# Kernel optimization log

Measured on AMD Instinct MI355X. Metric: run time of the kernel, lower is better.

## Reference

```python
import jax, jax.numpy as jnp
import numpy as np

LEAK = 0.2
N, C, T, H, DOUT = 512, 16, 15, 32, 32


def setup_inputs() -> dict:
    key = jax.random.key(0)
    k = jax.random.split(key, 5)
    x = jax.random.normal(k[0], (N, C), dtype=jnp.float32)
    adj = jax.random.uniform(k[1], (N, N, T), dtype=jnp.float32)
    W1 = jax.random.normal(k[2], (2 * C, T + 1, H), dtype=jnp.float32) * 0.05
    W2 = jax.random.normal(k[3], (2 * C, T + 1, DOUT), dtype=jnp.float32) * 0.05
    W3 = jax.random.normal(k[4], (C, H), dtype=jnp.float32) * 0.05
    return {"x": x, "adj": adj, "W1": W1, "W2": W2, "W3": W3}


def reference(x, adj, W1, W2, W3):
    n, c = x.shape
    # input_diag: [N,N,C,1], diagonal copy of node features
    diag = jnp.einsum('mn,ni->mni', jnp.eye(n, dtype=x.dtype), x)[..., None]
    # D = concat(adj-weighted broadcast of x, diag) along edge-type axis -> [N,N,C,T+1]
    D = jnp.concatenate([jnp.einsum('mnt,ni->mnit', adj, x), diag], axis=3)
    # symmetrize along channel axis -> [N,N,2C,T+1]
    D = jnp.concatenate([D, jnp.transpose(D, (1, 0, 2, 3))], axis=2)
    K = jnp.einsum('mnit,ith->mnh', D, W1)   # [N,N,H]
    V = jnp.einsum('mnit,itd->mnd', D, W2)   # [N,N,DOUT]
    Q = x @ W3                               # [N,H]
    logits1 = jnp.einsum('nh,nmh->nm', Q, K)
    logits2 = jnp.einsum('mh,nmh->nm', Q, K)
    s1 = jax.nn.softmax(logits1, axis=1)
    s2 = jax.nn.softmax(logits2, axis=0)
    temp = jnp.einsum('nm,nmd->nd', s1, V) + jnp.einsum('nm,nmd->md', s2, V)
    return jnp.maximum(temp, LEAK * temp)  # lrelu
```

## Files before the change

kernel.cpp:

```cpp
#include <hip/hip_runtime.h>
#include <hip/hip_bf16.h>

#define NNODE 512
#define CCH   16
#define TT    15
#define TP    16
#define HH    32
#define DD    32

typedef unsigned short u16;
typedef unsigned int   u32;
typedef short bf8 __attribute__((ext_vector_type(8)));
typedef float f4  __attribute__((ext_vector_type(4)));

__device__ __forceinline__ float bf2f(u16 v) {
    union { u32 u; float f; } x; x.u = ((u32)v) << 16; return x.f;
}
__device__ __forceinline__ u16 f2bf(float f) {
    union { float f; u32 u; } x; x.f = f;
    u32 u = x.u;
    return (u16)((u + 0x7FFFu + ((u >> 16) & 1u)) >> 16);
}
__device__ __forceinline__ void unpack8(uint4 p, float* o) {
    o[0]=bf2f((u16)(p.x & 0xffffu)); o[1]=bf2f((u16)(p.x >> 16));
    o[2]=bf2f((u16)(p.y & 0xffffu)); o[3]=bf2f((u16)(p.y >> 16));
    o[4]=bf2f((u16)(p.z & 0xffffu)); o[5]=bf2f((u16)(p.z >> 16));
    o[6]=bf2f((u16)(p.w & 0xffffu)); o[7]=bf2f((u16)(p.w >> 16));
}
__device__ __forceinline__ uint4 pack8(const u16* v) {
    return make_uint4((u32)v[0]|((u32)v[1]<<16), (u32)v[2]|((u32)v[3]<<16),
                      (u32)v[4]|((u32)v[5]<<16), (u32)v[6]|((u32)v[7]<<16));
}

__global__ __launch_bounds__(256) void k_prep_adjp(
    const float* __restrict__ x, const float* __restrict__ W1,
    const float* __restrict__ W2, const float* __restrict__ W3,
    const float* __restrict__ adj,
    u16* __restrict__ A1, u16* __restrict__ B1,
    u16* __restrict__ A2T, u16* __restrict__ B2T,
    u16* __restrict__ Qb, float* __restrict__ QAd, float* __restrict__ QB,
    u16* __restrict__ adjP, u16* __restrict__ adjPT)
{
    int tid = threadIdx.x;
    if (blockIdx.x < 512) {
        int n = blockIdx.x;
        __shared__ alignas(16) float xs[CCH];
        __shared__ alignas(16) float A1row[512], B1row[512];
        __shared__ alignas(16) float A2row[512], B2row[512];
        __shared__ alignas(16) float Qs[HH];
        if (tid < CCH) xs[tid] = x[n*CCH + tid];
        __syncthreads();
        float xr[CCH];
        #pragma unroll
        for (int i=0;i<CCH;i++) xr[i]=xs[i];
        #pragma unroll
        for (int rep=0; rep<2; rep++) {
            int c = tid + rep*256;
            float a1=0.f,b1=0.f,a2=0.f,b2=0.f;
            #pragma unroll
            for (int i=0;i<CCH;i++) {
                a1 += xr[i]*W1[i*512 + c];
                b1 += xr[i]*W1[(CCH+i)*512 + c];
                a2 += xr[i]*W2[i*512 + c];
                b2 += xr[i]*W2[(CCH+i)*512 + c];
            }
            A1[(size_t)n*512 + c]=f2bf(a1); B1[(size_t)n*512 + c]=f2bf(b1);
            A1row[c]=a1; B1row[c]=b1; A2row[c]=a2; B2row[c]=b2;
        }
        if (tid < HH) {
            float q=0.f;
            #pragma unroll
            for (int i=0;i<CCH;i++) q += xr[i]*W3[i*HH + tid];
            Qs[tid]=q; Qb[(size_t)n*HH + tid]=f2bf(q);
        }
        __syncthreads();
        if (tid < TP) {
            float qa=0.f, qb=0.f;
            #pragma unroll
            for (int h=0;h<HH;h++) { qa += Qs[h]*A1row[tid*HH+h]; qb += Qs[h]*B1row[tid*HH+h]; }
            QAd[(size_t)n*TP + tid]=qa; QB[(size_t)n*TP + tid]=qb;
        }
        {
            int d = tid >> 3, t0 = (tid & 7) * 2;
            u32 pa = (u32)f2bf(A2row[t0*32 + d]) | ((u32)f2bf(A2row[(t0+1)*32 + d]) << 16);
            u32 pb = (u32)f2bf(B2row[t0*32 + d]) | ((u32)f2bf(B2row[(t0+1)*32 + d]) << 16);
            *(u32*)(A2T + (size_t)d*8192 + n*16 + t0) = pa;
            *(u32*)(B2T + (size_t)d*8192 + n*16 + t0) = pb;
        }
    } else {
        int b = blockIdx.x - 512;
        int n0 = (b >> 4) * 32, m0 = (b & 15) * 32;
        __shared__ alignas(16) u16 s[32*520];
        #pragma unroll
        for (int i = 0; i < 60; i++) {
            int e = tid + i*256;
            int nl = e / 480; int rem = e - nl*480;
            int ml = rem / 15; int t = rem - ml*15;
            float v = adj[((size_t)(n0+nl)*512 + (m0+ml))*TT + t];
            s[nl*520 + ml*16 + t] = f2bf(v);
        }
        #pragma unroll
        for (int i = 0; i < 4; i++) {
            int e = tid + i*256; int nl = e >> 5, ml = e & 31;
            s[nl*520 + ml*16 + 15] = ((n0+nl) == (m0+ml)) ? (u16)0x3F80 : (u16)0;
        }
        __syncthreads();
        #pragma unroll
        for (int i = 0; i < 8; i++) {
            int c = tid + i*256;
            int nl = c >> 6, off = (c & 63) * 8;
            uint4 vv = *(const uint4*)(s + nl*520 + off);
            *(uint4*)(adjP + (size_t)(n0+nl)*8192 + m0*16 + off) = vv;
        }
        #pragma unroll
        for (int i = 0; i < 8; i++) {
            int c = tid + i*256;
            int ml = c >> 6, nlh = c & 63, nl = nlh >> 1, half = nlh & 1;
            uint4 vv = *(const uint4*)(s + nl*520 + ml*16 + half*8);
            *(uint4*)(adjPT + (size_t)(m0+ml)*8192 + (n0+nl)*16 + half*8) = vv;
        }
    }
}

__global__ __launch_bounds__(256) void k_logits(
    const u16* __restrict__ Qb, const u16* __restrict__ A1, const u16* __restrict__ B1,
    const u16* __restrict__ adjP, const u16* __restrict__ adjPT,
    const float* __restrict__ QAd, const float* __restrict__ QB,
    float* __restrict__ L1, float* __restrict__ L2T)
{
    const int m0 = blockIdx.x * 16, n0 = blockIdx.y * 16;
    const int tid = threadIdx.x;
    const int wv = tid >> 6, lane = tid & 63, l15 = lane & 15, quad = lane >> 4;
    __shared__ alignas(16) float sL1[16*17];
    __shared__ alignas(16) float sL2[16*17];

    bf8 qbN = *(const bf8*)(Qb + (size_t)(n0 + l15)*32 + quad*8);
    bf8 qbM = *(const bf8*)(Qb + (size_t)(m0 + l15)*32 + quad*8);
    float4 qb4 = *(const float4*)(QB  + (size_t)(n0 + l15)*TP + quad*4);
    float4 qa4 = *(const float4*)(QAd + (size_t)(m0 + l15)*TP + quad*4);

    #pragma unroll
    for (int j = 0; j < 4; j++) {
        int m = m0 + wv*4 + j;
        bf8 aA1 = *(const bf8*)(A1 + (size_t)m*512 + l15*32 + quad*8);
        f4 z = {0.f,0.f,0.f,0.f};
        f4 g = __builtin_amdgcn_mfma_f32_16x16x32_bf16(aA1, qbN, z, 0, 0, 0);
        uint2 ax = *(const uint2*)(adjPT + (size_t)m*8192 + (n0 + l15)*16 + quad*4);
        uint2 ay = *(const uint2*)(adjP  + (size_t)m*8192 + (n0 + l15)*16 + quad*4);
        float v;
        v = bf2f((u16)(ax.x & 0xffffu)) * g[0];
        v = fmaf(bf2f((u16)(ax.x >> 16)),     g[1], v);
        v = fmaf(bf2f((u16)(ax.y & 0xffffu)), g[2], v);
        v = fmaf(bf2f((u16)(ax.y >> 16)),     g[3], v);
        v = fmaf(bf2f((u16)(ay.x & 0xffffu)), qb4.x, v);
        v = fmaf(bf2f((u16)(ay.x >> 16)),     qb4.y, v);
        v = fmaf(bf2f((u16)(ay.y & 0xffffu)), qb4.z, v);
        v = fmaf(bf2f((u16)(ay.y >> 16)),     qb4.w, v);
        v += __shfl_xor(v, 16, 64);
        v += __shfl_xor(v, 32, 64);
        if (quad == 0) sL1[l15*17 + wv*4 + j] = v;
    }
    #pragma unroll
    for (int j = 0; j < 4; j++) {
        int n = n0 + wv*4 + j;
        bf8 aB1 = *(const bf8*)(B1 + (size_t)n*512 + l15*32 + quad*8);
        f4 z = {0.f,0.f,0.f,0.f};
        f4 h = __builtin_amdgcn_mfma_f32_16x16x32_bf16(aB1, qbM, z, 0, 0, 0);
        uint2 ax = *(const uint2*)(adjPT + (size_t)n*8192 + (m0 + l15)*16 + quad*4);
        uint2 ay = *(const uint2*)(adjP  + (size_t)n*8192 + (m0 + l15)*16 + quad*4);
        float v;
        v = bf2f((u16)(ax.x & 0xffffu)) * h[0];
        v = fmaf(bf2f((u16)(ax.x >> 16)),     h[1], v);
        v = fmaf(bf2f((u16)(ax.y & 0xffffu)), h[2], v);
        v = fmaf(bf2f((u16)(ax.y >> 16)),     h[3], v);
        v = fmaf(bf2f((u16)(ay.x & 0xffffu)), qa4.x, v);
        v = fmaf(bf2f((u16)(ay.x >> 16)),     qa4.y, v);
        v = fmaf(bf2f((u16)(ay.y & 0xffffu)), qa4.z, v);
        v = fmaf(bf2f((u16)(ay.y >> 16)),     qa4.w, v);
        v += __shfl_xor(v, 16, 64);
        v += __shfl_xor(v, 32, 64);
        if (quad == 0) sL2[l15*17 + wv*4 + j] = v;
    }
    __syncthreads();
    int row = tid >> 4, col = tid & 15;
    L1 [(size_t)(n0+row)*NNODE + m0 + col] = sL1[row*17+col];
    L2T[(size_t)(m0+row)*NNODE + n0 + col] = sL2[row*17+col];
}

__global__ __launch_bounds__(256) void k_smx_gemm(
    const float* __restrict__ L1, const float* __restrict__ L2T,
    const u16* __restrict__ adjP, const u16* __restrict__ adjPT,
    const u16* __restrict__ A2T, const u16* __restrict__ B2T,
    float* __restrict__ tempP2, float* __restrict__ uP)
{
    const int j0 = blockIdx.x * 16, kc = blockIdx.y, dir = blockIdx.z;
    const int tid = threadIdx.x;
    const int wv = tid >> 6, lane = tid & 63, l15 = lane & 15, quad = lane >> 4;
    const float* Lbase = dir ? L2T : L1;

    __shared__ alignas(16) u16 Wt[16*512];
    __shared__ alignas(16) float redb[4][512];
    __shared__ float mxs[16], invs[16];

    #pragma unroll
    for (int rr = 0; rr < 4; rr++) {
        int jr = wv*4 + rr;
        const float* rw = Lbase + (size_t)(j0 + jr)*NNODE;
        float4 a = *(const float4*)(rw + lane*8);
        float4 b = *(const float4*)(rw + lane*8 + 4);
        float mx = fmaxf(fmaxf(fmaxf(a.x,a.y),fmaxf(a.z,a.w)),
                         fmaxf(fmaxf(b.x,b.y),fmaxf(b.z,b.w)));
        #pragma unroll
        for (int o=32; o; o>>=1) mx = fmaxf(mx, __shfl_xor(mx, o, 64));
        float sm = __expf(a.x-mx)+__expf(a.y-mx)+__expf(a.z-mx)+__expf(a.w-mx)
                 + __expf(b.x-mx)+__expf(b.y-mx)+__expf(b.z-mx)+__expf(b.w-mx);
        #pragma unroll
        for (int o=32; o; o>>=1) sm += __shfl_xor(sm, o, 64);
        if (lane == 0) { mxs[jr] = mx; invs[jr] = 1.0f/sm; }
    }
    __syncthreads();

    {
        int j = tid >> 4, cb = tid & 15;
        float mxj = mxs[j], invj = invs[j];
        int mg = kc*32 + cb*2;
        const float* rw = Lbase + (size_t)(j0 + j)*NNODE;
        float s0 = __expf(rw[mg]   - mxj) * invj;
        float s1 = __expf(rw[mg+1] - mxj) * invj;

        const uint4* pp = (const uint4*)(adjP + (size_t)(j0+j)*8192 + kc*512 + cb*32);
        float av[32];
        unpack8(pp[0], av); unpack8(pp[1], av+8); unpack8(pp[2], av+16); unpack8(pp[3], av+24);
        u16 wo[32];
        #pragma unroll
        for (int e=0;e<16;e++) wo[e]    = f2bf(s0*av[e]);
        #pragma unroll
        for (int e=0;e<16;e++) wo[16+e] = f2bf(s1*av[16+e]);
        #pragma unroll
        for (int q=0;q<4;q++) {
            int sl = (cb*4 + q) ^ (j & 7);
            *(uint4*)&Wt[j*512 + sl*8] = pack8(wo + q*8);
        }

        const uint4* qq4 = (const uint4*)(adjPT + (size_t)(j0+j)*8192 + kc*512 + cb*32);
        float tv[32];
        unpack8(qq4[0], tv); unpack8(qq4[1], tv+8); unpack8(qq4[2], tv+16); unpack8(qq4[3], tv+24);
        float ut[16];
        #pragma unroll
        for (int t=0;t<16;t++) ut[t] = s0*tv[t] + s1*tv[16+t];
        #pragma unroll
        for (int i=0;i<8;i++) {
            float v0 = (lane&1) ? ut[i] : ut[i+8];
            float r0 = __shfl_xor(v0, 1, 64);
            ut[i] = ((lane&1) ? ut[i+8] : ut[i]) + r0;
        }
        #pragma unroll
        for (int i=0;i<4;i++) {
            float v0 = (lane&2) ? ut[i] : ut[i+4];
            float r0 = __shfl_xor(v0, 2, 64);
            ut[i] = ((lane&2) ? ut[i+4] : ut[i]) + r0;
        }
        #pragma unroll
        for (int i=0;i<2;i++) {
            float v0 = (lane&4) ? ut[i] : ut[i+2];
            float r0 = __shfl_xor(v0, 4, 64);
            ut[i] = ((lane&4) ? ut[i+2] : ut[i]) + r0;
        }
        {
            float v0 = (lane&8) ? ut[0] : ut[1];
            float r0 = __shfl_xor(v0, 8, 64);
            ut[0] = ((lane&8) ? ut[1] : ut[0]) + r0;
        }
        int tm = ((cb&1)<<3) | ((cb&2)<<1) | ((cb&4)>>1) | ((cb&8)>>3);
        uP[((size_t)(dir*16 + kc)*NNODE + j0 + j)*TP + tm] = ut[0];
    }
    __syncthreads();

    {
        const u16* Bmat = dir ? B2T : A2T;
        f4 acc0 = {0.f,0.f,0.f,0.f}, acc1 = {0.f,0.f,0.f,0.f};
        #pragma unroll
        for (int st = 0; st < 4; st++) {
            int s = wv*4 + st;
            bf8 afr = *(const bf8*)&Wt[l15*512 + (((s*4 + quad) ^ (l15 & 7)) << 3)];
            bf8 b0 = *(const bf8*)(Bmat + (size_t)(l15)*8192    + kc*512 + s*32 + quad*8);
            bf8 b1 = *(const bf8*)(Bmat + (size_t)(16+l15)*8192 + kc*512 + s*32 + quad*8);
            acc0 = __builtin_amdgcn_mfma_f32_16x16x32_bf16(afr, b0, acc0, 0, 0, 0);
            acc1 = __builtin_amdgcn_mfma_f32_16x16x32_bf16(afr, b1, acc1, 0, 0, 0);
        }
        #pragma unroll
        for (int r = 0; r < 4; r++) {
            redb[wv][      (quad*4+r)*16 + l15] = acc0[r];
            redb[wv][256 + (quad*4+r)*16 + l15] = acc1[r];
        }
    }
    __syncthreads();
    #pragma unroll
    for (int h = 0; h < 2; h++) {
        int o = tid + h*256;
        int jj = o >> 5, d = o & 31;
        int idx = (d >> 4)*256 + jj*16 + (d & 15);
        float v = redb[0][idx] + redb[1][idx] + redb[2][idx] + redb[3][idx];
        tempP2[(((size_t)dir*16 + kc)*NNODE + j0 + jj)*DD + d] = v;
    }
}

__global__ __launch_bounds__(256) void k_final(
    const float* __restrict__ tempP2, const float* __restrict__ uP,
    const u16* __restrict__ A2T, const u16* __restrict__ B2T, float* __restrict__ out)
{
    int blk = blockIdx.x, tid = threadIdx.x;
    int jbase = blk*8;
    __shared__ float u1L[8][16], v2L[8][16];
    {
        int dsel = tid >> 7;
        int i = tid & 127; int jj = i >> 4, t = i & 15;
        float s = 0.f;
        #pragma unroll
        for (int kcc = 0; kcc < 16; kcc++)
            s += uP[(((size_t)dsel*16 + kcc)*NNODE + jbase + jj)*TP + t];
        if (dsel) v2L[jj][t] = s; else u1L[jj][t] = s;
    }
    __syncthreads();
    int base = blk*256 + tid;
    int j = base >> 5, d = base & 31, jj = j & 7;
    float acc = 0.f;
    #pragma unroll
    for (int p = 0; p < 32; p++) acc += tempP2[((size_t)p*NNODE + j)*DD + d];
    const uint4* pb2 = (const uint4*)(B2T + (size_t)d*8192 + j*16);
    const uint4* pa2 = (const uint4*)(A2T + (size_t)d*8192 + j*16);
    float bv[16], avv[16];
    unpack8(pb2[0], bv);  unpack8(pb2[1], bv+8);
    unpack8(pa2[0], avv); unpack8(pa2[1], avv+8);
    #pragma unroll
    for (int t = 0; t < 16; t++)
        acc += u1L[jj][t]*bv[t] + v2L[jj][t]*avv[t];
    out[(size_t)j*DD + d] = fmaxf(acc, 0.2f*acc);
}

extern "C" void kernel_launch(void* const* d_in, const int* in_sizes, int n_in,
                              void* d_out, int out_size, void* d_ws, size_t ws_size,
                              hipStream_t stream)
{
    (void)in_sizes; (void)n_in; (void)out_size; (void)ws_size;
    const float* x   = (const float*)d_in[0];
    const float* adj = (const float*)d_in[1];
    const float* W1  = (const float*)d_in[2];
    const float* W2  = (const float*)d_in[3];
    const float* W3  = (const float*)d_in[4];

    char* ws = (char*)d_ws;
    u16*   adjP  = (u16*)(ws);
    u16*   adjPT = (u16*)(ws + 0x800000);
    u16*   A1    = (u16*)(ws + 0x1000000);
    u16*   B1    = (u16*)(ws + 0x1080000);
    u16*   A2T   = (u16*)(ws + 0x1100000);
    u16*   B2T   = (u16*)(ws + 0x1180000);
    u16*   Qb    = (u16*)(ws + 0x1200000);
    float* QAd   = (float*)(ws + 0x1210000);
    float* QB    = (float*)(ws + 0x1220000);
    float* L1    = (float*)(ws + 0x1300000);
    float* L2T   = (float*)(ws + 0x1400000);
    float* tempP2= (float*)(ws + 0x1500000);
    float* uP    = (float*)(ws + 0x1700000);

    k_prep_adjp<<<768, 256, 0, stream>>>(x, W1, W2, W3, adj,
                                         A1, B1, A2T, B2T, Qb, QAd, QB, adjP, adjPT);
    k_logits<<<dim3(32,32), 256, 0, stream>>>(Qb, A1, B1, adjP, adjPT, QAd, QB, L1, L2T);
    k_smx_gemm<<<dim3(32,16,2), 256, 0, stream>>>(L1, L2T, adjP, adjPT, A2T, B2T, tempP2, uP);
    k_final<<<64, 256, 0, stream>>>(tempP2, uP, A2T, B2T, (float*)d_out);
}
```

Measured before the change: 103.4 us.

## Split softmax stats into own kernel, double gemm grid, reduce partials with atomics

Moves the per-row softmax max and sum computation out of k_smx_gemm into a new k_stats kernel, which also zeroes the accumulators. k_smx_gemm then runs with half the K-chunk per block over twice as many blocks. Partial results are accumulated with float atomicAdd into temp/u1/v2, so k_final no longer sums 32 partial buffers. This removes redundant recomputation of row statistics in every block and the partial-sum reduction, at the cost of an extra launch, atomic contention, and non-deterministic summation order.

```diff
diff --git a/kernel.cpp b/kernel.cpp
--- a/kernel.cpp
+++ b/kernel.cpp
@@ -187,67 +187,75 @@
     L2T[(size_t)(m0+row)*NNODE + n0 + col] = sL2[row*17+col];
 }
 
+__global__ __launch_bounds__(256) void k_stats(
+    const float* __restrict__ L1, const float* __restrict__ L2T,
+    float2* __restrict__ stats, float* __restrict__ temp,
+    float* __restrict__ u1, float* __restrict__ v2)
+{
+    int tid = threadIdx.x;
+    int g0 = blockIdx.x * 256 + tid;
+    if (g0 < 16384) temp[g0] = 0.f;
+    else if (g0 < 24576) u1[g0 - 16384] = 0.f;
+    else if (g0 < 32768) v2[g0 - 24576] = 0.f;
+
+    int wv = tid >> 6, lane = tid & 63;
+    int g = blockIdx.x * 4 + wv;
+    const float* rw = (g < NNODE) ? (L1 + (size_t)g*NNODE)
+                                  : (L2T + (size_t)(g - NNODE)*NNODE);
+    float4 a = *(const float4*)(rw + lane*8);
+    float4 b = *(const float4*)(rw + lane*8 + 4);
+    float mx = fmaxf(fmaxf(fmaxf(a.x,a.y),fmaxf(a.z,a.w)),
+                     fmaxf(fmaxf(b.x,b.y),fmaxf(b.z,b.w)));
+    #pragma unroll
+    for (int o=32; o; o>>=1) mx = fmaxf(mx, __shfl_xor(mx, o, 64));
+    float sm = __expf(a.x-mx)+__expf(a.y-mx)+__expf(a.z-mx)+__expf(a.w-mx)
+             + __expf(b.x-mx)+__expf(b.y-mx)+__expf(b.z-mx)+__expf(b.w-mx);
+    #pragma unroll
+    for (int o=32; o; o>>=1) sm += __shfl_xor(sm, o, 64);
+    if (lane == 0) { float2 st; st.x = mx; st.y = 1.0f/sm; stats[g] = st; }
+}
+
 __global__ __launch_bounds__(256) void k_smx_gemm(
     const float* __restrict__ L1, const float* __restrict__ L2T,
     const u16* __restrict__ adjP, const u16* __restrict__ adjPT,
     const u16* __restrict__ A2T, const u16* __restrict__ B2T,
-    float* __restrict__ tempP2, float* __restrict__ uP)
+    const float2* __restrict__ stats,
+    float* __restrict__ temp, float* __restrict__ u1, float* __restrict__ v2)
 {
     const int j0 = blockIdx.x * 16, kc = blockIdx.y, dir = blockIdx.z;
     const int tid = threadIdx.x;
     const int wv = tid >> 6, lane = tid & 63, l15 = lane & 15, quad = lane >> 4;
     const float* Lbase = dir ? L2T : L1;
 
-    __shared__ alignas(16) u16 Wt[16*512];
+    __shared__ alignas(16) u16 Wt[16*256];
     __shared__ alignas(16) float redb[4][512];
-    __shared__ float mxs[16], invs[16];
-
-    #pragma unroll
-    for (int rr = 0; rr < 4; rr++) {
-        int jr = wv*4 + rr;
-        const float* rw = Lbase + (size_t)(j0 + jr)*NNODE;
-        float4 a = *(const float4*)(rw + lane*8);
-        float4 b = *(const float4*)(rw + lane*8 + 4);
-        float mx = fmaxf(fmaxf(fmaxf(a.x,a.y),fmaxf(a.z,a.w)),
-                         fmaxf(fmaxf(b.x,b.y),fmaxf(b.z,b.w)));
-        #pragma unroll
-        for (int o=32; o; o>>=1) mx = fmaxf(mx, __shfl_xor(mx, o, 64));
-        float sm = __expf(a.x-mx)+__expf(a.y-mx)+__expf(a.z-mx)+__expf(a.w-mx)
-                 + __expf(b.x-mx)+__expf(b.y-mx)+__expf(b.z-mx)+__expf(b.w-mx);
-        #pragma unroll
-        for (int o=32; o; o>>=1) sm += __shfl_xor(sm, o, 64);
-        if (lane == 0) { mxs[jr] = mx; invs[jr] = 1.0f/sm; }
-    }
+    __shared__ float2 sst[16];
+
+    if (tid < 16) sst[tid] = stats[dir*NNODE + j0 + tid];
     __syncthreads();
 
     {
         int j = tid >> 4, cb = tid & 15;
-        float mxj = mxs[j], invj = invs[j];
-        int mg = kc*32 + cb*2;
-        const float* rw = Lbase + (size_t)(j0 + j)*NNODE;
-        float s0 = __expf(rw[mg]   - mxj) * invj;
-        float s1 = __expf(rw[mg+1] - mxj) * invj;
-
-        const uint4* pp = (const uint4*)(adjP + (size_t)(j0+j)*8192 + kc*512 + cb*32);
-        float av[32];
-        unpack8(pp[0], av); unpack8(pp[1], av+8); unpack8(pp[2], av+16); unpack8(pp[3], av+24);
-        u16 wo[32];
-        #pragma unroll
-        for (int e=0;e<16;e++) wo[e]    = f2bf(s0*av[e]);
-        #pragma unroll
-        for (int e=0;e<16;e++) wo[16+e] = f2bf(s1*av[16+e]);
-        #pragma unroll
-        for (int q=0;q<4;q++) {
-            int sl = (cb*4 + q) ^ (j & 7);
-            *(uint4*)&Wt[j*512 + sl*8] = pack8(wo + q*8);
-        }
-
-        const uint4* qq4 = (const uint4*)(adjPT + (size_t)(j0+j)*8192 + kc*512 + cb*32);
-        float tv[32];
-        unpack8(qq4[0], tv); unpack8(qq4[1], tv+8); unpack8(qq4[2], tv+16); unpack8(qq4[3], tv+24);
+        int m = kc*16 + cb;
+        float2 st = sst[j];
+        float s0 = __expf(Lbase[(size_t)(j0+j)*NNODE + m] - st.x) * st.y;
+
+        const uint4* pp = (const uint4*)(adjP + (size_t)(j0+j)*8192 + m*16);
+        float av[16]; unpack8(pp[0], av); unpack8(pp[1], av+8);
+        u16 wo[16];
+        #pragma unroll
+        for (int e=0;e<16;e++) wo[e] = f2bf(s0*av[e]);
+        #pragma unroll
+        for (int q=0;q<2;q++) {
+            int sl = (cb*2 + q) ^ (j & 7);
+            *(uint4*)&Wt[j*256 + sl*8] = pack8(wo + q*8);
+        }
+
+        const uint4* qq = (const uint4*)(adjPT + (size_t)(j0+j)*8192 + m*16);
+        float tv[16]; unpack8(qq[0], tv); unpack8(qq[1], tv+8);
         float ut[16];
         #pragma unroll
-        for (int t=0;t<16;t++) ut[t] = s0*tv[t] + s1*tv[16+t];
+        for (int t=0;t<16;t++) ut[t] = s0*tv[t];
         #pragma unroll
         for (int i=0;i<8;i++) {
             float v0 = (lane&1) ? ut[i] : ut[i+8];
@@ -272,7 +280,7 @@
             ut[0] = ((lane&8) ? ut[1] : ut[0]) + r0;
         }
         int tm = ((cb&1)<<3) | ((cb&2)<<1) | ((cb&4)>>1) | ((cb&8)>>3);
-        uP[((size_t)(dir*16 + kc)*NNODE + j0 + j)*TP + tm] = ut[0];
+        atomicAdd((dir ? v2 : u1) + (size_t)(j0+j)*TP + tm, ut[0]);
     }
     __syncthreads();
 
@@ -280,11 +288,11 @@
         const u16* Bmat = dir ? B2T : A2T;
         f4 acc0 = {0.f,0.f,0.f,0.f}, acc1 = {0.f,0.f,0.f,0.f};
         #pragma unroll
-        for (int st = 0; st < 4; st++) {
-            int s = wv*4 + st;
-            bf8 afr = *(const bf8*)&Wt[l15*512 + (((s*4 + quad) ^ (l15 & 7)) << 3)];
-            bf8 b0 = *(const bf8*)(Bmat + (size_t)(l15)*8192    + kc*512 + s*32 + quad*8);
-            bf8 b1 = *(const bf8*)(Bmat + (size_t)(16+l15)*8192 + kc*512 + s*32 + quad*8);
+        for (int st2 = 0; st2 < 2; st2++) {
+            int s = wv*2 + st2;
+            bf8 afr = *(const bf8*)&Wt[l15*256 + (((s*4 + quad) ^ (l15 & 7)) << 3)];
+            bf8 b0 = *(const bf8*)(Bmat + (size_t)(l15)*8192    + kc*256 + s*32 + quad*8);
+            bf8 b1 = *(const bf8*)(Bmat + (size_t)(16+l15)*8192 + kc*256 + s*32 + quad*8);
             acc0 = __builtin_amdgcn_mfma_f32_16x16x32_bf16(afr, b0, acc0, 0, 0, 0);
             acc1 = __builtin_amdgcn_mfma_f32_16x16x32_bf16(afr, b1, acc1, 0, 0, 0);
         }
@@ -301,32 +309,17 @@
         int jj = o >> 5, d = o & 31;
         int idx = (d >> 4)*256 + jj*16 + (d & 15);
         float v = redb[0][idx] + redb[1][idx] + redb[2][idx] + redb[3][idx];
-        tempP2[(((size_t)dir*16 + kc)*NNODE + j0 + jj)*DD + d] = v;
+        atomicAdd(&temp[(size_t)(j0 + jj)*DD + d], v);
     }
 }
 
 __global__ __launch_bounds__(256) void k_final(
-    const float* __restrict__ tempP2, const float* __restrict__ uP,
+    const float* __restrict__ temp, const float* __restrict__ u1, const float* __restrict__ v2,
     const u16* __restrict__ A2T, const u16* __restrict__ B2T, float* __restrict__ out)
 {
-    int blk = blockIdx.x, tid = threadIdx.x;
-    int jbase = blk*8;
-    __shared__ float u1L[8][16], v2L[8][16];
-    {
-        int dsel = tid >> 7;
-        int i = tid & 127; int jj = i >> 4, t = i & 15;
-        float s = 0.f;
-        #pragma unroll
-        for (int kcc = 0; kcc < 16; kcc++)
-            s += uP[(((size_t)dsel*16 + kcc)*NNODE + jbase + jj)*TP + t];
-        if (dsel) v2L[jj][t] = s; else u1L[jj][t] = s;
-    }
-    __syncthreads();
-    int base = blk*256 + tid;
-    int j = base >> 5, d = base & 31, jj = j & 7;
-    float acc = 0.f;
-    #pragma unroll
-    for (int p = 0; p < 32; p++) acc += tempP2[((size_t)p*NNODE + j)*DD + d];
+    int base = blockIdx.x * 256 + threadIdx.x;
+    int j = base >> 5, d = base & 31;
+    float acc = temp[(size_t)j*DD + d];
     const uint4* pb2 = (const uint4*)(B2T + (size_t)d*8192 + j*16);
     const uint4* pa2 = (const uint4*)(A2T + (size_t)d*8192 + j*16);
     float bv[16], avv[16];
@@ -334,7 +327,7 @@
     unpack8(pa2[0], avv); unpack8(pa2[1], avv+8);
     #pragma unroll
     for (int t = 0; t < 16; t++)
-        acc += u1L[jj][t]*bv[t] + v2L[jj][t]*avv[t];
+        acc += u1[(size_t)j*TP + t]*bv[t] + v2[(size_t)j*TP + t]*avv[t];
     out[(size_t)j*DD + d] = fmaxf(acc, 0.2f*acc);
 }
 
@@ -361,12 +354,16 @@
     float* QB    = (float*)(ws + 0x1220000);
     float* L1    = (float*)(ws + 0x1300000);
     float* L2T   = (float*)(ws + 0x1400000);
-    float* tempP2= (float*)(ws + 0x1500000);
-    float* uP    = (float*)(ws + 0x1700000);
+    float* temp  = (float*)(ws + 0x1500000);
+    float* u1    = (float*)(ws + 0x1510000);
+    float* v2    = (float*)(ws + 0x1520000);
+    float2* stats= (float2*)(ws + 0x1530000);
 
     k_prep_adjp<<<768, 256, 0, stream>>>(x, W1, W2, W3, adj,
                                          A1, B1, A2T, B2T, Qb, QAd, QB, adjP, adjPT);
     k_logits<<<dim3(32,32), 256, 0, stream>>>(Qb, A1, B1, adjP, adjPT, QAd, QB, L1, L2T);
-    k_smx_gemm<<<dim3(32,16,2), 256, 0, stream>>>(L1, L2T, adjP, adjPT, A2T, B2T, tempP2, uP);
-    k_final<<<64, 256, 0, stream>>>(tempP2, uP, A2T, B2T, (float*)d_out);
-}
+    k_stats<<<256, 256, 0, stream>>>(L1, L2T, stats, temp, u1, v2);
+    k_smx_gemm<<<dim3(32,32,2), 256, 0, stream>>>(L1, L2T, adjP, adjPT, A2T, B2T,
+                                                  stats, temp, u1, v2);
+    k_final<<<64, 256, 0, stream>>>(temp, u1, v2, A2T, B2T, (float*)d_out);
+}
```

Result: no change. 103.2 us (-0.3%).
